# Performance work log

Hardware: AMD Instinct MI355X
Metric: run time of the kernel (lower is better)

The kernel has to match this reference:

```python
import jax, jax.numpy as jnp
import numpy as np
from functools import partial

N_OSC = 50
N_PER = 40
DT = 0.001
STEPS = 700
HALF_PI = float(np.pi / 2)
# limb constants (simple antagonist-muscle one-link limb, as in TorchOneLinkMuscleLimb)
R_MOM = 0.02      # muscle moment arm
L0 = 0.1          # muscle length at angle 0
INERTIA = 1e-3
DAMP = 0.01
K_MUS = 50.0
L_REST = 0.05
TAU_M = 0.05


def get_m1_length(theta):
    return L0 - R_MOM * theta


def get_m2_length(theta):
    return L0 + R_MOM * theta


def limb_f(l_state, activation):
    # l_state: (B,4) = (angle, ang. velocity, m1 length, m2 length); activation: (B,2)
    theta, omega, l1, l2 = l_state[:, 0], l_state[:, 1], l_state[:, 2], l_state[:, 3]
    f1 = jax.nn.relu(activation[:, 0]) * K_MUS * jax.nn.relu(l1 - L_REST)
    f2 = jax.nn.relu(activation[:, 1]) * K_MUS * jax.nn.relu(l2 - L_REST)
    domega = (R_MOM * (f2 - f1) - DAMP * omega) / INERTIA
    dl1 = (get_m1_length(theta) - l1) / TAU_M
    dl2 = (get_m2_length(theta) - l2) / TAU_M
    return jnp.stack([omega, domega, dl1, dl2], axis=1)


def setup_inputs() -> dict:
    key = jax.random.key(0)
    ks = jax.random.split(key, 16)
    B = 4096
    x = jax.random.normal(ks[0], (B, 2), dtype=jnp.float32) * 0.5
    def lin(k, out_d, in_d, scale=None):
        s = (1.0 / np.sqrt(in_d)) if scale is None else scale
        kw, kb = jax.random.split(k)
        w = jax.random.uniform(kw, (out_d, in_d), jnp.float32, -s, s)
        b = jax.random.uniform(kb, (out_d,), jnp.float32, -s, s)
        return w, b
    fc1_w, fc1_b = lin(ks[1], 128, 2)
    fc2_w, fc2_b = lin(ks[2], 128, 128)
    fc3_w, fc3_b = lin(ks[3], N_OSC * 2, 128)
    fcd_w, fcd_b = lin(ks[4], 2, 128)
    fcd_w = fcd_w / 100.0
    fcd_b = fcd_b * 0.0 + 0.1
    fc4_w, fc4_b = lin(ks[5], 32, N_OSC * N_PER)
    fc5_w, fc5_b = lin(ks[6], 2, 32)
    fc5_w = fc5_w / 10000.0
    fc5_b = fc5_b * 0.0
    # NEF oscillator populations: encoders (unit vectors), biases, decoders
    enc = jax.random.normal(ks[7], (N_OSC, N_PER, 2), dtype=jnp.float32)
    enc = enc / jnp.linalg.norm(enc, axis=-1, keepdims=True)
    osc_bias = jax.random.uniform(ks[8], (N_OSC, N_PER), jnp.float32, -1.0, 1.0)
    dec = jax.random.normal(ks[9], (N_OSC, 2, N_PER), dtype=jnp.float32) * 0.05
    return dict(x=x, fc1_w=fc1_w, fc1_b=fc1_b, fc2_w=fc2_w, fc2_b=fc2_b,
                fc3_w=fc3_w, fc3_b=fc3_b, fcd_w=fcd_w, fcd_b=fcd_b,
                enc=enc, osc_bias=osc_bias, dec=dec,
                fc4_w=fc4_w, fc4_b=fc4_b, fc5_w=fc5_w, fc5_b=fc5_b)


def _forward(x, fc1_w, fc1_b, fc2_w, fc2_b, fc3_w, fc3_b, fcd_w, fcd_b,
             enc, osc_bias, dec, fc4_w, fc4_b, fc5_w, fc5_b):
    B = x.shape[0]
    current_angle = x[:, 0]
    h = jax.nn.relu(x @ fc1_w.T + fc1_b)
    direct = h @ fcd_w.T + fcd_b                     # (B, 2)
    h2 = jax.nn.relu(h @ fc2_w.T + fc2_b)
    xo = h2 @ fc3_w.T + fc3_b                        # (B, 2*N_OSC)
    o0 = jnp.transpose(xo.reshape(B, N_OSC, 2), (1, 0, 2))   # (O, B, 2)
    l0 = jnp.stack([current_angle, jnp.zeros_like(current_angle),
                    get_m1_length(current_angle), get_m2_length(current_angle)], axis=1)

    def step(carry, _):
        o_states, l_state = carry
        # NEF activities: relu(encoders . state + bias) per oscillator
        a = jax.nn.relu(jnp.einsum('opd,obd->obp', enc, o_states) + osc_bias[:, None, :])  # (O,B,P)
        deriv = jnp.einsum('odp,obp->obd', dec, a)
        o_states = o_states + DT * deriv
        activities = jnp.transpose(a, (1, 0, 2)).reshape(B, N_OSC * N_PER)  # (B, 2000)
        b1 = jax.nn.relu(activities @ fc4_w.T + fc4_b)
        activation = b1 @ fc5_w.T + fc5_b + direct    # (B, 2)
        l_new = l_state + DT * limb_f(l_state, activation)
        pos, vel = l_new[:, 0], l_new[:, 1]
        in_bounds = (pos > -HALF_PI) & (pos < HALF_PI)
        l_new = jnp.stack([jnp.clip(pos, -HALF_PI, HALF_PI),
                           jnp.where(in_bounds, vel, 0.0),
                           l_new[:, 2], l_new[:, 3]], axis=1)
        return (o_states, l_new), (l_new, activation)

    (_, _), (l_states, activations) = jax.lax.scan(step, (o0, l0), None, length=STEPS)
    return l_states, activations


@jax.jit
def reference(x, fc1_w, fc1_b, fc2_w, fc2_b, fc3_w, fc3_b, fcd_w, fcd_b,
              enc, osc_bias, dec, fc4_w, fc4_b, fc5_w, fc5_b):
    return _forward(x, fc1_w, fc1_b, fc2_w, fc2_b, fc3_w, fc3_b, fcd_w, fcd_b,
                    enc, osc_bias, dec, fc4_w, fc4_b, fc5_w, fc5_b)
```

## Files before the change

kernel.cpp:

```cpp
#include <hip/hip_runtime.h>

#define NTHR 1024
#define NB   16
#define NOSC 50
#define NPER 40
#define KTOT 2000
#define KPAD 2048
#define NSTEP 700
#define BATCH 4096
#define B1STR 36
#define HALF_PI 1.57079632679489662f
#define ACT_OFF ((size_t)NSTEP * BATCH * 4)

typedef _Float16 v8h __attribute__((ext_vector_type(8)));
typedef _Float16 h2_t __attribute__((ext_vector_type(2)));
typedef float v4f __attribute__((ext_vector_type(4)));

__device__ _Float16 g_w4[32 * KPAD];

__device__ __forceinline__ float fdot2f(float a_bits, float b_bits, float acc) {
    h2_t a = __builtin_bit_cast(h2_t, a_bits);
    h2_t b = __builtin_bit_cast(h2_t, b_bits);
#if __has_builtin(__builtin_amdgcn_fdot2)
    return __builtin_amdgcn_fdot2(a, b, acc, false);
#else
    return fmaf((float)a[0], (float)b[0], fmaf((float)a[1], (float)b[1], acc));
#endif
}

__device__ __forceinline__ float dot4(float4 a, float4 b, float acc) {
    acc = fmaf(a.x, b.x, acc);
    acc = fmaf(a.y, b.y, acc);
    acc = fmaf(a.z, b.z, acc);
    acc = fmaf(a.w, b.w, acc);
    return acc;
}

__device__ __forceinline__ float pkrtz(float a, float b) {
    auto q = __builtin_amdgcn_cvt_pkrtz(a, b);
    return __builtin_bit_cast(float, q);
}

__device__ __forceinline__ float cvt2rtn(float a, float b) {
    h2_t u; u[0] = (_Float16)a; u[1] = (_Float16)b;
    return __builtin_bit_cast(float, u);
}

__global__ void prep_f16(const float* __restrict__ fc4_w) {
    int tid = blockIdx.x * blockDim.x + threadIdx.x;
    int j = tid >> 11, k = tid & 2047;
    g_w4[j * KPAD + k] = (k < KTOT) ? (_Float16)fc4_w[j * KTOT + k] : (_Float16)0.f;
}

__global__ __launch_bounds__(NTHR)
__attribute__((amdgpu_waves_per_eu(4, 4)))
void net_main(const float* __restrict__ x,
              const float* __restrict__ fc1_w, const float* __restrict__ fc1_b,
              const float* __restrict__ fc2_w, const float* __restrict__ fc2_b,
              const float* __restrict__ fc3_w, const float* __restrict__ fc3_b,
              const float* __restrict__ fcd_w, const float* __restrict__ fcd_b,
              const float* __restrict__ enc,   const float* __restrict__ osc_bias,
              const float* __restrict__ dec,
              const float* __restrict__ fc4_b,
              const float* __restrict__ fc5_w, const float* __restrict__ fc5_b,
              float* __restrict__ out)
{
    __shared__ __align__(16) _Float16 act_sh[256 * 128];
    __shared__ __align__(16) float part[16 * 2 * 256];
    __shared__ __align__(16) float os_sh[NOSC * NB * 2];
    __shared__ __align__(16) float b1s[NB * B1STR];
    __shared__ __align__(16) float dir[NB * 2];

    const int t    = threadIdx.x;
    const int lane = t & 63;
    const int wv   = t >> 6;
    const int b0   = blockIdx.x * NB;

    float* h  = (float*)act_sh;
    float* h2 = (float*)act_sh + NB * 128;

    #pragma unroll
    for (int ii = 0; ii < 2; ++ii) {
        int task = t + ii * NTHR;
        int b = task >> 7, i = task & 127;
        float x0 = x[(b0 + b) * 2 + 0];
        float x1 = x[(b0 + b) * 2 + 1];
        float v = fmaf(x0, fc1_w[2 * i], fmaf(x1, fc1_w[2 * i + 1], fc1_b[i]));
        h[b * 128 + i] = fmaxf(v, 0.f);
    }
    __syncthreads();
    #pragma unroll
    for (int ii = 0; ii < 2; ++ii) {
        int task = t + ii * NTHR;
        int b = task >> 7, i = task & 127;
        float acc = fc2_b[i];
        #pragma unroll 4
        for (int k = 0; k < 128; k += 4)
            acc = dot4(*(const float4*)&fc2_w[i * 128 + k],
                       *(const float4*)&h[b * 128 + k], acc);
        h2[b * 128 + i] = fmaxf(acc, 0.f);
    }
    if (t < NB * 2) {
        int b = t >> 1, j = t & 1;
        float acc = fcd_b[j];
        #pragma unroll 4
        for (int k = 0; k < 128; k += 4)
            acc = dot4(*(const float4*)&fcd_w[j * 128 + k],
                       *(const float4*)&h[b * 128 + k], acc);
        dir[b * 2 + j] = acc;
    }
    __syncthreads();
    #pragma unroll
    for (int ii = 0; ii < 2; ++ii) {
        int task = t + ii * NTHR;
        if (task < NOSC * NB * 2) {
            int o = task >> 5, r = task & 31, b = r >> 1;
            int row = o * 2 + (r & 1);
            float acc = fc3_b[row];
            #pragma unroll 4
            for (int k = 0; k < 128; k += 4)
                acc = dot4(*(const float4*)&fc3_w[row * 128 + k],
                           *(const float4*)&h2[b * 128 + k], acc);
            os_sh[o * 32 + r] = acc;
        }
    }
    const int my_oct = t >> 2;
    float4 e0 = {0,0,0,0}, e1 = {0,0,0,0}, e2 = {0,0,0,0}, e3 = {0,0,0,0};
    float4 bi0 = {0,0,0,0}, bi1 = {0,0,0,0};
    int my_o = 0;
    if (my_oct < 250) {
        const float4* ep = (const float4*)&enc[my_oct * 16];
        e0 = ep[0]; e1 = ep[1]; e2 = ep[2]; e3 = ep[3];
        const float4* bp = (const float4*)&osc_bias[my_oct * 8];
        bi0 = bp[0]; bi1 = bp[1];
        my_o = my_oct / 5;
    }
    float4 dd0[5], dd1[5];
    if (t < NOSC * NB) {
        int o = t >> 4;
        const float* d0p = &dec[(o * 2 + 0) * 40];
        const float* d1p = &dec[(o * 2 + 1) * 40];
        #pragma unroll
        for (int c = 0; c < 5; ++c) {
            dd0[c].x = cvt2rtn(d0p[c*8+0], d0p[c*8+1]);
            dd0[c].y = cvt2rtn(d0p[c*8+2], d0p[c*8+3]);
            dd0[c].z = cvt2rtn(d0p[c*8+4], d0p[c*8+5]);
            dd0[c].w = cvt2rtn(d0p[c*8+6], d0p[c*8+7]);
            dd1[c].x = cvt2rtn(d1p[c*8+0], d1p[c*8+1]);
            dd1[c].y = cvt2rtn(d1p[c*8+2], d1p[c*8+3]);
            dd1[c].z = cvt2rtn(d1p[c*8+4], d1p[c*8+5]);
            dd1[c].w = cvt2rtn(d1p[c*8+6], d1p[c*8+7]);
        }
    }
    float theta = 0.f, omega = 0.f, l1 = 0.f, l2 = 0.f, bs0 = 0.f, bs1 = 0.f;
    const int cb = t - 960;
    if (cb >= 0 && cb < NB) {
        theta = x[(b0 + cb) * 2 + 0];
        l1 = fmaf(-0.02f, theta, 0.1f);
        l2 = fmaf( 0.02f, theta, 0.1f);
    }
    __syncthreads();
    if (cb >= 0 && cb < NB) {
        bs0 = dir[cb * 2 + 0] + fc5_b[0];
        bs1 = dir[cb * 2 + 1] + fc5_b[1];
    }
    if (t < 768) act_sh[32000 + t] = (_Float16)0.f;

    const int n_col = lane & 15, quad = lane >> 4;
    const int lidx  = lane ^ (quad << 2);
    int a_off[4];
    #pragma unroll
    for (int ks4 = 0; ks4 < 4; ++ks4) {
        int oct = (wv * 4 + ks4) * 4 + quad;
        a_off[ks4] = oct * 128 + ((n_col ^ (oct & 15)) * 8);
    }
    v8h wr[8];
    {
        const _Float16* wp = &g_w4[n_col * KPAD + wv * 128 + quad * 8];
        #pragma unroll
        for (int ks4 = 0; ks4 < 4; ++ks4) {
            wr[ks4]     = *(const v8h*)&wp[ks4 * 32];
            wr[4 + ks4] = *(const v8h*)&wp[16 * KPAD + ks4 * 32];
        }
    }

    auto phaseA = [&]() {
        if (my_oct < 250) {
            const int i4 = (t & 3) << 2;
            float4 osA = *(const float4*)&os_sh[my_o * 32 + i4 * 2];
            float4 osB = *(const float4*)&os_sh[my_o * 32 + i4 * 2 + 4];
            #pragma unroll
            for (int ii = 0; ii < 4; ++ii) {
                int b = i4 + ii;
                float osx = (ii == 0) ? osA.x : (ii == 1) ? osA.z : (ii == 2) ? osB.x : osB.z;
                float osy = (ii == 0) ? osA.y : (ii == 1) ? osA.w : (ii == 2) ? osB.y : osB.w;
                float r0 = fmaxf(fmaf(e0.x, osx, fmaf(e0.y, osy, bi0.x)), 0.f);
                float r1 = fmaxf(fmaf(e0.z, osx, fmaf(e0.w, osy, bi0.y)), 0.f);
                float r2 = fmaxf(fmaf(e1.x, osx, fmaf(e1.y, osy, bi0.z)), 0.f);
                float r3 = fmaxf(fmaf(e1.z, osx, fmaf(e1.w, osy, bi0.w)), 0.f);
                float r4 = fmaxf(fmaf(e2.x, osx, fmaf(e2.y, osy, bi1.x)), 0.f);
                float r5 = fmaxf(fmaf(e2.z, osx, fmaf(e2.w, osy, bi1.y)), 0.f);
                float r6 = fmaxf(fmaf(e3.x, osx, fmaf(e3.y, osy, bi1.z)), 0.f);
                float r7 = fmaxf(fmaf(e3.z, osx, fmaf(e3.w, osy, bi1.w)), 0.f);
                float4 pk;
                pk.x = pkrtz(r0, r1);
                pk.y = pkrtz(r2, r3);
                pk.z = pkrtz(r4, r5);
                pk.w = pkrtz(r6, r7);
                *(float4*)&act_sh[my_oct * 128 + ((b ^ my_oct) & 15) * 8] = pk;
            }
        }
    };

    phaseA();
    __syncthreads();

    for (int s = 0; s < NSTEP; ++s) {
        {
            v4f c0 = {0.f, 0.f, 0.f, 0.f}, c1 = {0.f, 0.f, 0.f, 0.f};
            #pragma unroll
            for (int ks4 = 0; ks4 < 4; ++ks4) {
                v8h a = *(const v8h*)&act_sh[a_off[ks4]];
                c0 = __builtin_amdgcn_mfma_f32_16x16x32_f16(a, wr[ks4],     c0, 0, 0, 0);
                c1 = __builtin_amdgcn_mfma_f32_16x16x32_f16(a, wr[4 + ks4], c1, 0, 0, 0);
            }
            *(v4f*)&part[(wv * 2 + 0) * 256 + lidx * 4] = c0;
            *(v4f*)&part[(wv * 2 + 1) * 256 + lidx * 4] = c1;
        }
        if (t < NOSC * NB) {
            int o = t >> 4, b = t & 15;
            float p0 = 0.f, p1 = 0.f, q0 = 0.f, q1 = 0.f;
            #pragma unroll
            for (int c = 0; c < 5; ++c) {
                int oct = o * 5 + c;
                float4 af = *(const float4*)&act_sh[oct * 128 + ((b ^ oct) & 15) * 8];
                p0 = fdot2f(af.x, dd0[c].x, p0); p1 = fdot2f(af.y, dd0[c].y, p1);
                p0 = fdot2f(af.z, dd0[c].z, p0); p1 = fdot2f(af.w, dd0[c].w, p1);
                q0 = fdot2f(af.x, dd1[c].x, q0); q1 = fdot2f(af.y, dd1[c].y, q1);
                q0 = fdot2f(af.z, dd1[c].z, q0); q1 = fdot2f(af.w, dd1[c].w, q1);
            }
            float2 osv = *(const float2*)&os_sh[o * 32 + b * 2];
            osv.x += 0.001f * (p0 + p1);
            osv.y += 0.001f * (q0 + q1);
            *(float2*)&os_sh[o * 32 + b * 2] = osv;
        } else if (cb >= 0 && cb < NB && s > 0) {
            float a0 = bs0, a1 = bs1;
            #pragma unroll
            for (int i = 0; i < 32; i += 4) {
                float4 bv = *(const float4*)&b1s[cb * B1STR + i];
                a0 = dot4(bv, *(const float4*)&fc5_w[i],      a0);
                a1 = dot4(bv, *(const float4*)&fc5_w[32 + i], a1);
            }
            float f1v = fmaxf(a0, 0.f) * 50.f * fmaxf(l1 - 0.05f, 0.f);
            float f2v = fmaxf(a1, 0.f) * 50.f * fmaxf(l2 - 0.05f, 0.f);
            float domega = (0.02f * (f2v - f1v) - 0.01f * omega) / 0.001f;
            float dl1 = ((0.1f - 0.02f * theta) - l1) / 0.05f;
            float dl2 = ((0.1f + 0.02f * theta) - l2) / 0.05f;
            float pos = fmaf(0.001f, omega,  theta);
            float vel = fmaf(0.001f, domega, omega);
            l1 = fmaf(0.001f, dl1, l1);
            l2 = fmaf(0.001f, dl2, l2);
            bool inb = (pos > -HALF_PI) && (pos < HALF_PI);
            float posc = fminf(fmaxf(pos, -HALF_PI), HALF_PI);
            vel = inb ? vel : 0.f;
            theta = posc;
            omega = vel;
            float4 lo; lo.x = posc; lo.y = vel; lo.z = l1; lo.w = l2;
            *(float4*)&out[((size_t)(s - 1) * BATCH + (b0 + cb)) * 4] = lo;
            float2 ao; ao.x = a0; ao.y = a1;
            *(float2*)&out[ACT_OFF + ((size_t)(s - 1) * BATCH + (b0 + cb)) * 2] = ao;
        }
        __syncthreads();

        if (t < 512) {
            int b = t & 15, j = t >> 4;
            int g = j >> 4, n = j & 15;
            int Lp = (b >> 2) * 16 + (n ^ ((b >> 2) << 2));
            int base = g * 256 + Lp * 4 + (b & 3);
            float sum = 0.f;
            #pragma unroll
            for (int w = 0; w < 16; ++w)
                sum += part[w * 512 + base];
            b1s[b * B1STR + j] = fmaxf(sum + fc4_b[j], 0.f);
        }
        phaseA();
        __syncthreads();
    }

    if (cb >= 0 && cb < NB) {
        const int s = NSTEP - 1;
        float a0 = bs0, a1 = bs1;
        #pragma unroll
        for (int i = 0; i < 32; i += 4) {
            float4 bv = *(const float4*)&b1s[cb * B1STR + i];
            a0 = dot4(bv, *(const float4*)&fc5_w[i],      a0);
            a1 = dot4(bv, *(const float4*)&fc5_w[32 + i], a1);
        }
        float f1v = fmaxf(a0, 0.f) * 50.f * fmaxf(l1 - 0.05f, 0.f);
        float f2v = fmaxf(a1, 0.f) * 50.f * fmaxf(l2 - 0.05f, 0.f);
        float domega = (0.02f * (f2v - f1v) - 0.01f * omega) / 0.001f;
        float dl1 = ((0.1f - 0.02f * theta) - l1) / 0.05f;
        float dl2 = ((0.1f + 0.02f * theta) - l2) / 0.05f;
        float pos = fmaf(0.001f, omega,  theta);
        float vel = fmaf(0.001f, domega, omega);
        l1 = fmaf(0.001f, dl1, l1);
        l2 = fmaf(0.001f, dl2, l2);
        bool inb = (pos > -HALF_PI) && (pos < HALF_PI);
        float posc = fminf(fmaxf(pos, -HALF_PI), HALF_PI);
        vel = inb ? vel : 0.f;
        float4 lo; lo.x = posc; lo.y = vel; lo.z = l1; lo.w = l2;
        *(float4*)&out[((size_t)s * BATCH + (b0 + cb)) * 4] = lo;
        float2 ao; ao.x = a0; ao.y = a1;
        *(float2*)&out[ACT_OFF + ((size_t)s * BATCH + (b0 + cb)) * 2] = ao;
    }
}

extern "C" void kernel_launch(void* const* d_in, const int* in_sizes, int n_in,
                              void* d_out, int out_size, void* d_ws, size_t ws_size,
                              hipStream_t stream) {
    (void)in_sizes; (void)n_in; (void)d_ws; (void)ws_size; (void)out_size;
    const float* x_     = (const float*)d_in[0];
    const float* fc1_w  = (const float*)d_in[1];
    const float* fc1_b  = (const float*)d_in[2];
    const float* fc2_w  = (const float*)d_in[3];
    const float* fc2_b  = (const float*)d_in[4];
    const float* fc3_w  = (const float*)d_in[5];
    const float* fc3_b  = (const float*)d_in[6];
    const float* fcd_w  = (const float*)d_in[7];
    const float* fcd_b  = (const float*)d_in[8];
    const float* enc    = (const float*)d_in[9];
    const float* oscb   = (const float*)d_in[10];
    const float* dec    = (const float*)d_in[11];
    const float* fc4_w  = (const float*)d_in[12];
    const float* fc4_b  = (const float*)d_in[13];
    const float* fc5_w  = (const float*)d_in[14];
    const float* fc5_b  = (const float*)d_in[15];
    float* out = (float*)d_out;

    hipLaunchKernelGGL(prep_f16, dim3(256), dim3(256), 0, stream, fc4_w);
    hipLaunchKernelGGL(net_main, dim3(BATCH / NB), dim3(NTHR), 0, stream,
                       x_, fc1_w, fc1_b, fc2_w, fc2_b, fc3_w, fc3_b,
                       fcd_w, fcd_b, enc, oscb, dec, fc4_b,
                       fc5_w, fc5_b, out);
}
```

Baseline: 2.059 ms.

## Halve batch per block to 8 and stage decoder weights in LDS

Each block now handles 8 batch rows with 512 threads instead of 16 rows with 1024. That doubles the grid and lets more blocks share each CU, which is meant to hide the per-step sync and latency chain of the 700-step loop. The per-thread work mapping, swizzled activation layout and partial-sum reduction are reworked to match. Each wave now issues twice as many MFMAs over a wider K slice, and the 16-row MFMA tiles carry duplicated batch rows, so matrix work per sample roughly doubles. Decoder weights move from per-thread fp16 registers into a shared fp16 array, which frees registers but adds LDS reads every step.

```diff
diff --git a/kernel.cpp b/kernel.cpp
--- a/kernel.cpp
+++ b/kernel.cpp
@@ -1,7 +1,7 @@
 #include <hip/hip_runtime.h>
 
-#define NTHR 1024
-#define NB   16
+#define NTHR 512
+#define NB   8
 #define NOSC 50
 #define NPER 40
 #define KTOT 2000
@@ -39,11 +39,6 @@
 __device__ __forceinline__ float pkrtz(float a, float b) {
     auto q = __builtin_amdgcn_cvt_pkrtz(a, b);
     return __builtin_bit_cast(float, q);
-}
-
-__device__ __forceinline__ float cvt2rtn(float a, float b) {
-    h2_t u; u[0] = (_Float16)a; u[1] = (_Float16)b;
-    return __builtin_bit_cast(float, u);
 }
 
 __global__ void prep_f16(const float* __restrict__ fc4_w) {
@@ -65,9 +60,10 @@
               const float* __restrict__ fc5_w, const float* __restrict__ fc5_b,
               float* __restrict__ out)
 {
-    __shared__ __align__(16) _Float16 act_sh[256 * 128];
-    __shared__ __align__(16) float part[16 * 2 * 256];
+    __shared__ __align__(16) _Float16 act_sh[256 * 64];
+    __shared__ __align__(16) float part[8 * 2 * 256];
     __shared__ __align__(16) float os_sh[NOSC * NB * 2];
+    __shared__ __align__(16) _Float16 dec_sh[4096];
     __shared__ __align__(16) float b1s[NB * B1STR];
     __shared__ __align__(16) float dir[NB * 2];
 
@@ -78,6 +74,8 @@
 
     float* h  = (float*)act_sh;
     float* h2 = (float*)act_sh + NB * 128;
+
+    for (int i = t; i < 4000; i += NTHR) dec_sh[i] = (_Float16)dec[i];
 
     #pragma unroll
     for (int ii = 0; ii < 2; ++ii) {
@@ -114,17 +112,17 @@
     for (int ii = 0; ii < 2; ++ii) {
         int task = t + ii * NTHR;
         if (task < NOSC * NB * 2) {
-            int o = task >> 5, r = task & 31, b = r >> 1;
+            int o = task >> 4, r = task & 15, b = r >> 1;
             int row = o * 2 + (r & 1);
             float acc = fc3_b[row];
             #pragma unroll 4
             for (int k = 0; k < 128; k += 4)
                 acc = dot4(*(const float4*)&fc3_w[row * 128 + k],
                            *(const float4*)&h2[b * 128 + k], acc);
-            os_sh[o * 32 + r] = acc;
-        }
-    }
-    const int my_oct = t >> 2;
+            os_sh[o * 16 + r] = acc;
+        }
+    }
+    const int my_oct = t >> 1;
     float4 e0 = {0,0,0,0}, e1 = {0,0,0,0}, e2 = {0,0,0,0}, e3 = {0,0,0,0};
     float4 bi0 = {0,0,0,0}, bi1 = {0,0,0,0};
     int my_o = 0;
@@ -135,25 +133,8 @@
         bi0 = bp[0]; bi1 = bp[1];
         my_o = my_oct / 5;
     }
-    float4 dd0[5], dd1[5];
-    if (t < NOSC * NB) {
-        int o = t >> 4;
-        const float* d0p = &dec[(o * 2 + 0) * 40];
-        const float* d1p = &dec[(o * 2 + 1) * 40];
-        #pragma unroll
-        for (int c = 0; c < 5; ++c) {
-            dd0[c].x = cvt2rtn(d0p[c*8+0], d0p[c*8+1]);
-            dd0[c].y = cvt2rtn(d0p[c*8+2], d0p[c*8+3]);
-            dd0[c].z = cvt2rtn(d0p[c*8+4], d0p[c*8+5]);
-            dd0[c].w = cvt2rtn(d0p[c*8+6], d0p[c*8+7]);
-            dd1[c].x = cvt2rtn(d1p[c*8+0], d1p[c*8+1]);
-            dd1[c].y = cvt2rtn(d1p[c*8+2], d1p[c*8+3]);
-            dd1[c].z = cvt2rtn(d1p[c*8+4], d1p[c*8+5]);
-            dd1[c].w = cvt2rtn(d1p[c*8+6], d1p[c*8+7]);
-        }
-    }
     float theta = 0.f, omega = 0.f, l1 = 0.f, l2 = 0.f, bs0 = 0.f, bs1 = 0.f;
-    const int cb = t - 960;
+    const int cb = t - 504;
     if (cb >= 0 && cb < NB) {
         theta = x[(b0 + cb) * 2 + 0];
         l1 = fmaf(-0.02f, theta, 0.1f);
@@ -164,31 +145,32 @@
         bs0 = dir[cb * 2 + 0] + fc5_b[0];
         bs1 = dir[cb * 2 + 1] + fc5_b[1];
     }
-    if (t < 768) act_sh[32000 + t] = (_Float16)0.f;
+    if (t < 384) act_sh[16000 + t] = (_Float16)0.f;
 
     const int n_col = lane & 15, quad = lane >> 4;
+    const int nc8   = n_col & 7;
     const int lidx  = lane ^ (quad << 2);
-    int a_off[4];
+    int a_off[8];
     #pragma unroll
-    for (int ks4 = 0; ks4 < 4; ++ks4) {
-        int oct = (wv * 4 + ks4) * 4 + quad;
-        a_off[ks4] = oct * 128 + ((n_col ^ (oct & 15)) * 8);
-    }
-    v8h wr[8];
+    for (int ks = 0; ks < 8; ++ks) {
+        int oct = (wv * 8 + ks) * 4 + quad;
+        a_off[ks] = oct * 64 + ((nc8 ^ (oct & 7)) * 8);
+    }
+    v8h wr[16];
     {
-        const _Float16* wp = &g_w4[n_col * KPAD + wv * 128 + quad * 8];
+        const _Float16* wp = &g_w4[n_col * KPAD + wv * 256 + quad * 8];
         #pragma unroll
-        for (int ks4 = 0; ks4 < 4; ++ks4) {
-            wr[ks4]     = *(const v8h*)&wp[ks4 * 32];
-            wr[4 + ks4] = *(const v8h*)&wp[16 * KPAD + ks4 * 32];
+        for (int ks = 0; ks < 8; ++ks) {
+            wr[ks]     = *(const v8h*)&wp[ks * 32];
+            wr[8 + ks] = *(const v8h*)&wp[16 * KPAD + ks * 32];
         }
     }
 
     auto phaseA = [&]() {
         if (my_oct < 250) {
-            const int i4 = (t & 3) << 2;
-            float4 osA = *(const float4*)&os_sh[my_o * 32 + i4 * 2];
-            float4 osB = *(const float4*)&os_sh[my_o * 32 + i4 * 2 + 4];
+            const int i4 = (t & 1) << 2;
+            float4 osA = *(const float4*)&os_sh[my_o * 16 + i4 * 2];
+            float4 osB = *(const float4*)&os_sh[my_o * 16 + i4 * 2 + 4];
             #pragma unroll
             for (int ii = 0; ii < 4; ++ii) {
                 int b = i4 + ii;
@@ -207,7 +189,7 @@
                 pk.y = pkrtz(r2, r3);
                 pk.z = pkrtz(r4, r5);
                 pk.w = pkrtz(r6, r7);
-                *(float4*)&act_sh[my_oct * 128 + ((b ^ my_oct) & 15) * 8] = pk;
+                *(float4*)&act_sh[my_oct * 64 + ((b ^ my_oct) & 7) * 8] = pk;
             }
         }
     };
@@ -219,30 +201,34 @@
         {
             v4f c0 = {0.f, 0.f, 0.f, 0.f}, c1 = {0.f, 0.f, 0.f, 0.f};
             #pragma unroll
-            for (int ks4 = 0; ks4 < 4; ++ks4) {
-                v8h a = *(const v8h*)&act_sh[a_off[ks4]];
-                c0 = __builtin_amdgcn_mfma_f32_16x16x32_f16(a, wr[ks4],     c0, 0, 0, 0);
-                c1 = __builtin_amdgcn_mfma_f32_16x16x32_f16(a, wr[4 + ks4], c1, 0, 0, 0);
+            for (int ks = 0; ks < 8; ++ks) {
+                v8h a = *(const v8h*)&act_sh[a_off[ks]];
+                c0 = __builtin_amdgcn_mfma_f32_16x16x32_f16(a, wr[ks],     c0, 0, 0, 0);
+                c1 = __builtin_amdgcn_mfma_f32_16x16x32_f16(a, wr[8 + ks], c1, 0, 0, 0);
             }
             *(v4f*)&part[(wv * 2 + 0) * 256 + lidx * 4] = c0;
             *(v4f*)&part[(wv * 2 + 1) * 256 + lidx * 4] = c1;
         }
         if (t < NOSC * NB) {
-            int o = t >> 4, b = t & 15;
+            int o = t >> 3, b = t & 7;
+            const _Float16* dr0 = &dec_sh[(o * 2 + 0) * 40];
+            const _Float16* dr1 = &dec_sh[(o * 2 + 1) * 40];
             float p0 = 0.f, p1 = 0.f, q0 = 0.f, q1 = 0.f;
             #pragma unroll
             for (int c = 0; c < 5; ++c) {
                 int oct = o * 5 + c;
-                float4 af = *(const float4*)&act_sh[oct * 128 + ((b ^ oct) & 15) * 8];
-                p0 = fdot2f(af.x, dd0[c].x, p0); p1 = fdot2f(af.y, dd0[c].y, p1);
-                p0 = fdot2f(af.z, dd0[c].z, p0); p1 = fdot2f(af.w, dd0[c].w, p1);
-                q0 = fdot2f(af.x, dd1[c].x, q0); q1 = fdot2f(af.y, dd1[c].y, q1);
-                q0 = fdot2f(af.z, dd1[c].z, q0); q1 = fdot2f(af.w, dd1[c].w, q1);
+                float4 af = *(const float4*)&act_sh[oct * 64 + ((b ^ oct) & 7) * 8];
+                float4 d0 = *(const float4*)&dr0[c * 8];
+                float4 d1 = *(const float4*)&dr1[c * 8];
+                p0 = fdot2f(af.x, d0.x, p0); p1 = fdot2f(af.y, d0.y, p1);
+                p0 = fdot2f(af.z, d0.z, p0); p1 = fdot2f(af.w, d0.w, p1);
+                q0 = fdot2f(af.x, d1.x, q0); q1 = fdot2f(af.y, d1.y, q1);
+                q0 = fdot2f(af.z, d1.z, q0); q1 = fdot2f(af.w, d1.w, q1);
             }
-            float2 osv = *(const float2*)&os_sh[o * 32 + b * 2];
+            float2 osv = *(const float2*)&os_sh[o * 16 + b * 2];
             osv.x += 0.001f * (p0 + p1);
             osv.y += 0.001f * (q0 + q1);
-            *(float2*)&os_sh[o * 32 + b * 2] = osv;
+            *(float2*)&os_sh[o * 16 + b * 2] = osv;
         } else if (cb >= 0 && cb < NB && s > 0) {
             float a0 = bs0, a1 = bs1;
             #pragma unroll
@@ -272,14 +258,15 @@
         }
         __syncthreads();
 
-        if (t < 512) {
-            int b = t & 15, j = t >> 4;
+        if (t < 256) {
+            int b = t & 7, j = t >> 3;
             int g = j >> 4, n = j & 15;
-            int Lp = (b >> 2) * 16 + (n ^ ((b >> 2) << 2));
+            int q = b >> 2;
+            int Lp = q * 16 + (n ^ (q << 2));
             int base = g * 256 + Lp * 4 + (b & 3);
             float sum = 0.f;
             #pragma unroll
-            for (int w = 0; w < 16; ++w)
+            for (int w = 0; w < 8; ++w)
                 sum += part[w * 512 + base];
             b1s[b * B1STR + j] = fmaxf(sum + fc4_b[j], 0.f);
         }
```

Result: slower. 2.404 ms (+16.7%).
